# Kernel optimization log

Hardware: AMD Instinct MI355X
Metric: run time of the kernel (lower is better)

Reference implementation:

```python
import jax, jax.numpy as jnp
import numpy as np
from jax import lax

V, D, H = 32000, 512, 512  # vocab, embedding_dim, hidden_size (must match for the DxD matmul chain)
B, T, A = 64, 256, 4       # batch, sentence len, aspect len
EPS = 1e-5


def setup_inputs() -> dict:
    key = jax.random.key(0)
    ks = jax.random.split(key, 12)
    sc = 0.05
    return {
        "x": jax.random.randint(ks[0], (B, T), 0, V),
        "s": jax.random.randint(ks[1], (B, A), 0, V),
        "embed": jax.random.normal(ks[2], (V, D), jnp.float32) * sc,
        "W_ih": jax.random.normal(ks[3], (4 * H, D), jnp.float32) * sc,
        "W_hh": jax.random.normal(ks[4], (4 * H, H), jnp.float32) * sc,
        "b_lstm": jax.random.normal(ks[5], (4 * H,), jnp.float32) * sc,
        "w_y": jax.random.normal(ks[6], (D, D), jnp.float32) * sc,
        "w_t": jax.random.normal(ks[7], (D, D), jnp.float32) * sc,
        "w_p": jax.random.normal(ks[8], (D, D), jnp.float32) * sc,
        "w_x": jax.random.normal(ks[9], (D, D), jnp.float32) * sc,
        "w_f": jax.random.normal(ks[10], (D, D), jnp.float32) * sc,
        "b_f": jax.random.normal(ks[11], (D,), jnp.float32) * sc,
    }


def _lstm(emb, W_ih, W_hh, b):
    # emb: [B, T, D] -> hidden states [B, T, H]; PyTorch gate order i,f,g,o
    Bx = emb.shape[0]
    Hh = W_hh.shape[1]
    h0 = jnp.zeros((Bx, Hh), emb.dtype)
    c0 = jnp.zeros((Bx, Hh), emb.dtype)

    def step(carry, x_t):
        h, c = carry
        z = x_t @ W_ih.T + h @ W_hh.T + b  # [B, 4H]
        i, f, g, o = jnp.split(z, 4, axis=-1)
        c = jax.nn.sigmoid(f) * c + jax.nn.sigmoid(i) * jnp.tanh(g)
        h = jax.nn.sigmoid(o) * jnp.tanh(c)
        return (h, c), h

    _, hs = lax.scan(step, (h0, c0), jnp.swapaxes(emb, 0, 1))
    return jnp.swapaxes(hs, 0, 1)  # [B, T, H]


def reference(x, s, embed, W_ih, W_hh, b_lstm, w_y, w_t, w_p, w_x, w_f, b_f):
    # 1) embed + LSTM over the sentence
    emb = embed[x]                      # [B, T, D]
    Hs = _lstm(emb, W_ih, W_hh, b_lstm)  # [B, T, H]

    # 2) aspect: embed, batch-normalize per feature, sum over aspect tokens
    s_emb = embed[s]                    # [B, A, D]
    mu = s_emb.mean(axis=(0, 1))
    var = s_emb.var(axis=(0, 1))
    s_norm = ((s_emb - mu) * lax.rsqrt(var + EPS)).sum(axis=1)  # [B, D]

    # 3) FFT circular correlation: m_t = ifft(fft(h_t) * conj(fft(s))).real
    Hf = jnp.fft.fft(Hs, axis=-1)                      # [B, T, D] complex
    Sf = jnp.conj(jnp.fft.fft(s_norm, axis=-1))        # [B, D]
    m = jnp.fft.ifft(Hf * Sf[:, None, :], axis=-1).real.astype(Hs.dtype)  # [B, T, D]

    # 4) attention chain
    Y = jnp.tanh(jnp.einsum('de,bte->btd', w_y, m))            # [B, T, D]
    alpha = jax.nn.softmax(jnp.einsum('de,bte->btd', w_t, Y), axis=1)  # softmax over time
    r = jnp.einsum('btd,btd->bd', alpha, Hs)                   # [B, D]
    h_star = jnp.tanh(r @ w_p.T + Hs[:, -1] @ w_x.T)           # [B, D]
    return jax.nn.softmax(h_star @ w_f.T + b_f, axis=-1)       # [B, D]
```

## Files before the change

### kernel.cpp

```cpp
#include <hip/hip_runtime.h>


typedef __bf16 bf16x8 __attribute__((ext_vector_type(8)));
typedef float f32x4 __attribute__((ext_vector_type(4)));

#define B_ 64
#define T_ 256
#define D_ 512
#define H4 2048

__device__ __forceinline__ unsigned short f2bf(float f) {
    unsigned u = __float_as_uint(f);
    u += 0x7fffu + ((u >> 16) & 1u);
    return (unsigned short)(u >> 16);
}
__device__ __forceinline__ float bf2f(unsigned short x) {
    return __uint_as_float(((unsigned)x) << 16);
}
__device__ __forceinline__ float bf2f_lo(unsigned u) { return __uint_as_float(u << 16); }
__device__ __forceinline__ float bf2f_hi(unsigned u) { return __uint_as_float(u & 0xffff0000u); }

__device__ __forceinline__ float frcp(float x) { return __builtin_amdgcn_rcpf(x); }
__device__ __forceinline__ float fast_sigmoid(float x) {
    return frcp(1.f + __expf(-x));
}
__device__ __forceinline__ float fast_tanh(float x) {
    return 1.f - 2.f * frcp(1.f + __expf(2.f * x));
}

__global__ __launch_bounds__(256)
void prep_kernel(const int* __restrict__ x,
                 const int* __restrict__ s,
                 const float* __restrict__ embed,
                 const float* __restrict__ Wih,
                 const float* __restrict__ wy,
                 const float* __restrict__ wt,
                 unsigned short* __restrict__ Wcat,
                 unsigned short* __restrict__ Ebf,
                 uint4* __restrict__ Hs4,
                 float* __restrict__ s_norm,
                 int use_ebf)
{
    __shared__ int sidx[256];
    const int bid = blockIdx.x;
    const int tid = threadIdx.x;

    if (bid < 2048) {
        const int i = (bid * 256 + tid) * 2;
        uint4 v = {0xFFFFFFFFu, 0xFFFFFFFFu, 0xFFFFFFFFu, 0xFFFFFFFFu};
        Hs4[i] = v;
        Hs4[i + 1] = v;
    } else if (bid < 3584) {
        const int i = ((bid - 2048) * 256 + tid) * 4;
        const float* src; int off;
        if (i < 1048576)      { src = Wih; off = 0; }
        else if (i < 1310720) { src = wy;  off = 1048576; }
        else                  { src = wt;  off = 1310720; }
        float4 v = *(const float4*)(src + (i - off));
        unsigned short o[4] __attribute__((aligned(8)));
        o[0] = f2bf(v.x); o[1] = f2bf(v.y); o[2] = f2bf(v.z); o[3] = f2bf(v.w);
        *(unsigned long long*)(Wcat + i) = *(const unsigned long long*)o;
    } else if (bid < 7680) {
        if (!use_ebf) return;
        const long i = ((long)(bid - 3584) * 256 + tid) * 8;
        const int row = (int)(i >> 9);
        const int col = (int)(i & 511);
        const float* src = embed + (long)x[row] * 512 + col;
        float4 u0 = *(const float4*)(src);
        float4 u1 = *(const float4*)(src + 4);
        unsigned short o[8] __attribute__((aligned(16)));
        o[0] = f2bf(u0.x); o[1] = f2bf(u0.y); o[2] = f2bf(u0.z); o[3] = f2bf(u0.w);
        o[4] = f2bf(u1.x); o[5] = f2bf(u1.y); o[6] = f2bf(u1.z); o[7] = f2bf(u1.w);
        *(uint4*)(Ebf + i) = *(const uint4*)o;
    } else {
        const int d = (bid - 7680) * 256 + tid;
        sidx[tid] = s[tid];
        __syncthreads();
        float sum = 0.f, sq = 0.f;
        for (int i = 0; i < 256; i++) {
            float v = embed[(long)sidx[i] * D_ + d];
            sum += v; sq += v * v;
        }
        float mu = sum * (1.f / 256.f);
        float var = sq * (1.f / 256.f) - mu * mu;
        float rstd = rsqrtf(var + 1e-5f);
        for (int b = 0; b < 64; b++) {
            float acc = 0.f;
            #pragma unroll
            for (int a = 0; a < 4; a++) {
                acc += embed[(long)sidx[b * 4 + a] * D_ + d] - mu;
            }
            s_norm[b * D_ + d] = acc * rstd;
        }
    }
}

__global__ __launch_bounds__(256)
void gemm_bt(const void* __restrict__ Abase, int a_f32,
             const int* __restrict__ gather_idx,
             const unsigned short* __restrict__ Bmat_h,
             const float* __restrict__ circ_src,
             const float* __restrict__ bias,
             unsigned short* __restrict__ outb,
             float* __restrict__ outf,
             int N, int K,
             long A_bstride, long out_bstride,
             int act)
{
    __shared__ __align__(16) unsigned short Asm[128 * 40];
    __shared__ __align__(16) unsigned short Bsm[128 * 40];

    const int bz = blockIdx.z;
    const int tile_n = blockIdx.x * 128;
    const int tile_m = blockIdx.y * 128;
    const int tid = threadIdx.x;
    const int lane = tid & 63;
    const int w = tid >> 6;
    const int wm = (w >> 1) * 64;
    const int wn = (w & 1) * 64;

    const int srow = tid >> 1;
    const int skc = (tid & 1) * 16;

    const float* arow_f = nullptr;
    const unsigned short* arow_h = nullptr;
    if (a_f32) {
        const float* Af = (const float*)Abase;
        if (gather_idx) arow_f = Af + (long)gather_idx[tile_m + srow] * K;
        else            arow_f = Af + (long)bz * A_bstride + (long)(tile_m + srow) * K;
    } else {
        arow_h = (const unsigned short*)Abase + (long)bz * A_bstride + (long)(tile_m + srow) * K;
    }
    const unsigned short* brow_h = nullptr;
    const float* csrc = nullptr;
    if (circ_src) csrc = circ_src + bz * 512;
    else brow_h = Bmat_h + (long)(tile_n + srow) * K;

    f32x4 zero4 = {0.f, 0.f, 0.f, 0.f};
    f32x4 acc[4][4];
    #pragma unroll
    for (int mi = 0; mi < 4; mi++)
        #pragma unroll
        for (int ni = 0; ni < 4; ni++) acc[mi][ni] = zero4;

    const int fr = lane & 15;
    const int fq = (lane >> 4) * 8;

    for (int kc = 0; kc < K; kc += 32) {
        __syncthreads();
        if (a_f32) {
            float4 u0 = *(const float4*)(arow_f + kc + skc);
            float4 u1 = *(const float4*)(arow_f + kc + skc + 4);
            float4 u2 = *(const float4*)(arow_f + kc + skc + 8);
            float4 u3 = *(const float4*)(arow_f + kc + skc + 12);
            unsigned short tmp[16] __attribute__((aligned(16)));
            tmp[0] = f2bf(u0.x); tmp[1] = f2bf(u0.y); tmp[2]  = f2bf(u0.z); tmp[3]  = f2bf(u0.w);
            tmp[4] = f2bf(u1.x); tmp[5] = f2bf(u1.y); tmp[6]  = f2bf(u1.z); tmp[7]  = f2bf(u1.w);
            tmp[8] = f2bf(u2.x); tmp[9] = f2bf(u2.y); tmp[10] = f2bf(u2.z); tmp[11] = f2bf(u2.w);
            tmp[12] = f2bf(u3.x); tmp[13] = f2bf(u3.y); tmp[14] = f2bf(u3.z); tmp[15] = f2bf(u3.w);
            *(uint4*)&Asm[srow * 40 + skc]     = *(const uint4*)tmp;
            *(uint4*)&Asm[srow * 40 + skc + 8] = *(const uint4*)(tmp + 8);
        } else {
            *(uint4*)&Asm[srow * 40 + skc]     = *(const uint4*)(arow_h + kc + skc);
            *(uint4*)&Asm[srow * 40 + skc + 8] = *(const uint4*)(arow_h + kc + skc + 8);
        }
        if (csrc) {
            unsigned short tmp[16] __attribute__((aligned(16)));
            int n_abs = tile_n + srow;
            #pragma unroll
            for (int j = 0; j < 16; j++) {
                int k_abs = kc + skc + j;
                tmp[j] = f2bf(csrc[(k_abs - n_abs) & 511]);
            }
            *(uint4*)&Bsm[srow * 40 + skc]     = *(const uint4*)tmp;
            *(uint4*)&Bsm[srow * 40 + skc + 8] = *(const uint4*)(tmp + 8);
        } else {
            *(uint4*)&Bsm[srow * 40 + skc]     = *(const uint4*)(brow_h + kc + skc);
            *(uint4*)&Bsm[srow * 40 + skc + 8] = *(const uint4*)(brow_h + kc + skc + 8);
        }
        __syncthreads();
        bf16x8 av[4], bv[4];
        #pragma unroll
        for (int mi = 0; mi < 4; mi++)
            av[mi] = *(const bf16x8*)&Asm[(wm + mi * 16 + fr) * 40 + fq];
        #pragma unroll
        for (int ni = 0; ni < 4; ni++)
            bv[ni] = *(const bf16x8*)&Bsm[(wn + ni * 16 + fr) * 40 + fq];
        #pragma unroll
        for (int mi = 0; mi < 4; mi++)
            #pragma unroll
            for (int ni = 0; ni < 4; ni++)
                acc[mi][ni] = __builtin_amdgcn_mfma_f32_16x16x32_bf16(
                    av[mi], bv[ni], acc[mi][ni], 0, 0, 0);
    }

    #pragma unroll
    for (int mi = 0; mi < 4; mi++) {
        #pragma unroll
        for (int ni = 0; ni < 4; ni++) {
            #pragma unroll
            for (int rg = 0; rg < 4; rg++) {
                int row = tile_m + wm + mi * 16 + (lane >> 4) * 4 + rg;
                int col = tile_n + wn + ni * 16 + (lane & 15);
                float v = acc[mi][ni][rg];
                if (bias) v += bias[col];
                if (act == 1) v = fast_tanh(v);
                long oidx = (long)bz * out_bstride + (long)row * N + col;
                if (outb) outb[oidx] = f2bf(v);
                else outf[oidx] = v;
            }
        }
    }
}

#define WSTRIDE 520
#define SENT 0xFFFFFFFFu
#define ZL(g,r,d) zl[((g)*8+(r))*65+(d)]

__global__ __launch_bounds__(512, 2)
void persistent_lstm(const float* __restrict__ Whh,
                     const unsigned short* __restrict__ Zx,
                     unsigned int* __restrict__ Hsu)
{
    __shared__ __align__(16) unsigned short hsm[16 * WSTRIDE];
    __shared__ float zl[4 * 8 * 65];

    const int cq  = blockIdx.x & 7;
    const int nbp = blockIdx.x >> 3;
    const int tid = threadIdx.x;
    const int w = tid >> 6;
    const int lane = tid & 63;
    const int fr = lane & 15;
    const int fq = (lane >> 4) * 8;
    const int g = w >> 1;
    const int f = w & 1;

    bf16x8 wfrag[2][16];
    #pragma unroll
    for (int n = 0; n < 2; n++) {
        const float* wrow = Whh + (long)(g * 512 + nbp * 64 + f * 32 + n * 16 + fr) * 512;
        #pragma unroll
        for (int c = 0; c < 16; c++) {
            int k0 = c * 32 + fq;
            float4 u0 = *(const float4*)(wrow + k0);
            float4 u1 = *(const float4*)(wrow + k0 + 4);
            unsigned short tmp[8] __attribute__((aligned(16)));
            tmp[0] = f2bf(u0.x); tmp[1] = f2bf(u0.y); tmp[2] = f2bf(u0.z); tmp[3] = f2bf(u0.w);
            tmp[4] = f2bf(u1.x); tmp[5] = f2bf(u1.y); tmp[6] = f2bf(u1.z); tmp[7] = f2bf(u1.w);
            wfrag[n][c] = *(const bf16x8*)tmp;
        }
    }

    for (int i = tid; i < 16 * WSTRIDE / 2; i += 512)
        ((unsigned*)hsm)[i] = 0;

    int st_r[4], st_dp[4];
    #pragma unroll
    for (int k = 0; k < 4; k++) {
        int idx = k * 512 + tid;
        st_r[k] = idx >> 8;
        st_dp[k] = idx & 255;
    }

    const int grow = (tid & 255) >> 5;
    const int d0 = (tid & 31) * 2;
    const int b_own = cq * 8 + grow;
    const int dg = nbp * 64 + d0;
    float ca = 0.f, cb = 0.f;

    f32x4 zero4 = {0.f, 0.f, 0.f, 0.f};

    for (int t = 0; t < T_; t++) {
        unsigned zi_u = 0, zf_u = 0, zg_u = 0, zo_u = 0;
        if (tid < 256) {
            const long zb = ((long)b_own * T_ + t) * H4 + dg;
            zi_u = *(const unsigned*)&Zx[zb + 0 * 512];
            zf_u = *(const unsigned*)&Zx[zb + 1 * 512];
            zg_u = *(const unsigned*)&Zx[zb + 2 * 512];
            zo_u = *(const unsigned*)&Zx[zb + 3 * 512];
        }

        f32x4 an0 = zero4, an1 = zero4;
        if (t > 0) {
            unsigned vv[4];
            long ad[4];
            #pragma unroll
            for (int k = 0; k < 4; k++) {
                ad[k] = ((long)(cq * 8 + st_r[k]) * T_ + (t - 1)) * 256 + st_dp[k];
                vv[k] = __hip_atomic_load(Hsu + ad[k], __ATOMIC_RELAXED,
                                          __HIP_MEMORY_SCOPE_AGENT);
            }
            while (true) {
                bool pend = false;
                #pragma unroll
                for (int k = 0; k < 4; k++) pend |= (vv[k] == SENT);
                if (!__ballot(pend)) break;
                #pragma unroll
                for (int k = 0; k < 4; k++) {
                    vv[k] = __hip_atomic_load(Hsu + ad[k], __ATOMIC_RELAXED,
                                              __HIP_MEMORY_SCOPE_AGENT);
                }
            }
            #pragma unroll
            for (int k = 0; k < 4; k++) {
                *(unsigned*)&hsm[st_r[k] * WSTRIDE + st_dp[k] * 2] = vv[k];
            }
            __syncthreads();
            const unsigned short* arow = hsm + fr * WSTRIDE;
            f32x4 a0[4] = {zero4, zero4, zero4, zero4};
            f32x4 a1[4] = {zero4, zero4, zero4, zero4};
            #pragma unroll
            for (int c = 0; c < 16; c += 4) {
                bf16x8 x0 = *(const bf16x8*)(arow + (c + 0) * 32 + fq);
                bf16x8 x1 = *(const bf16x8*)(arow + (c + 1) * 32 + fq);
                bf16x8 x2 = *(const bf16x8*)(arow + (c + 2) * 32 + fq);
                bf16x8 x3 = *(const bf16x8*)(arow + (c + 3) * 32 + fq);
                a0[0] = __builtin_amdgcn_mfma_f32_16x16x32_bf16(x0, wfrag[0][c + 0], a0[0], 0, 0, 0);
                a0[1] = __builtin_amdgcn_mfma_f32_16x16x32_bf16(x1, wfrag[0][c + 1], a0[1], 0, 0, 0);
                a0[2] = __builtin_amdgcn_mfma_f32_16x16x32_bf16(x2, wfrag[0][c + 2], a0[2], 0, 0, 0);
                a0[3] = __builtin_amdgcn_mfma_f32_16x16x32_bf16(x3, wfrag[0][c + 3], a0[3], 0, 0, 0);
                a1[0] = __builtin_amdgcn_mfma_f32_16x16x32_bf16(x0, wfrag[1][c + 0], a1[0], 0, 0, 0);
                a1[1] = __builtin_amdgcn_mfma_f32_16x16x32_bf16(x1, wfrag[1][c + 1], a1[1], 0, 0, 0);
                a1[2] = __builtin_amdgcn_mfma_f32_16x16x32_bf16(x2, wfrag[1][c + 2], a1[2], 0, 0, 0);
                a1[3] = __builtin_amdgcn_mfma_f32_16x16x32_bf16(x3, wfrag[1][c + 3], a1[3], 0, 0, 0);
            }
            an0 = (a0[0] + a0[1]) + (a0[2] + a0[3]);
            an1 = (a1[0] + a1[1]) + (a1[2] + a1[3]);
        }
        if (lane < 32) {
            const int rb = (lane >> 4) * 4;
            const int cl = f * 32 + (lane & 15);
            #pragma unroll
            for (int rg = 0; rg < 4; rg++) {
                ZL(g, rb + rg, cl)      = an0[rg];
                ZL(g, rb + rg, cl + 16) = an1[rg];
            }
        }
        __syncthreads();
        if (tid < 256) {
            float zi0 = ZL(0, grow, d0)     + bf2f_lo(zi_u);
            float zi1 = ZL(0, grow, d0 + 1) + bf2f_hi(zi_u);
            float zf0 = ZL(1, grow, d0)     + bf2f_lo(zf_u);
            float zf1 = ZL(1, grow, d0 + 1) + bf2f_hi(zf_u);
            float zg0 = ZL(2, grow, d0)     + bf2f_lo(zg_u);
            float zg1 = ZL(2, grow, d0 + 1) + bf2f_hi(zg_u);
            float zo0 = ZL(3, grow, d0)     + bf2f_lo(zo_u);
            float zo1 = ZL(3, grow, d0 + 1) + bf2f_hi(zo_u);

            ca = fast_sigmoid(zf0) * ca + fast_sigmoid(zi0) * fast_tanh(zg0);
            cb = fast_sigmoid(zf1) * cb + fast_sigmoid(zi1) * fast_tanh(zg1);
            float h0 = fast_sigmoid(zo0) * fast_tanh(ca);
            float h1 = fast_sigmoid(zo1) * fast_tanh(cb);

            unsigned hp = (unsigned)f2bf(h0) | ((unsigned)f2bf(h1) << 16);
            __hip_atomic_store(Hsu + ((long)b_own * T_ + t) * 256 + nbp * 32 + (tid & 31),
                               hp, __ATOMIC_RELAXED, __HIP_MEMORY_SCOPE_AGENT);
        }
    }
}

__global__ __launch_bounds__(256)
void tail_kernel(const float* __restrict__ apre,
                 const unsigned short* __restrict__ Hs,
                 const float* __restrict__ w_p,
                 const float* __restrict__ w_x,
                 const float* __restrict__ w_f,
                 const float* __restrict__ b_f,
                 float* __restrict__ out)
{
    __shared__ __align__(16) float apc[16 * 512];
    __shared__ __align__(16) unsigned short hc[16 * 512];
    __shared__ float rs[512];
    __shared__ float hts[512];
    __shared__ float hsr[512];
    __shared__ float lg[512];
    __shared__ float red[8];

    const int b = blockIdx.x, tid = threadIdx.x;
    const int d1 = tid + 256;
    const float* apb = apre + (long)b * T_ * D_;
    const unsigned short* hpb = Hs + (long)b * T_ * D_;

    float mx0 = -3.0e38f, sm0 = 0.f, ac0 = 0.f;
    float mx1 = -3.0e38f, sm1 = 0.f, ac1 = 0.f;

    for (int t0 = 0; t0 < T_; t0 += 16) {
        __syncthreads();
        for (int idx = tid; idx < 16 * 128; idx += 256) {
            int rr = idx >> 7, cc = (idx & 127) * 4;
            *(float4*)&apc[rr * 512 + cc] = *(const float4*)(apb + (long)(t0 + rr) * 512 + cc);
        }
        for (int idx = tid; idx < 16 * 64; idx += 256) {
            int rr = idx >> 6, cc = (idx & 63) * 8;
            *(uint4*)&hc[rr * 512 + cc] = *(const uint4*)(hpb + (long)(t0 + rr) * 512 + cc);
        }
        __syncthreads();
        #pragma unroll
        for (int i = 0; i < 16; i++) {
            float v0 = apc[i * 512 + tid];
            float h0 = bf2f(hc[i * 512 + tid]);
            if (v0 > mx0) {
                float fct = __expf(mx0 - v0);
                sm0 = sm0 * fct + 1.f;
                ac0 = ac0 * fct + h0;
                mx0 = v0;
            } else {
                float e = __expf(v0 - mx0);
                sm0 += e;
                ac0 += e * h0;
            }
            float v1 = apc[i * 512 + d1];
            float h1 = bf2f(hc[i * 512 + d1]);
            if (v1 > mx1) {
                float fct = __expf(mx1 - v1);
                sm1 = sm1 * fct + 1.f;
                ac1 = ac1 * fct + h1;
                mx1 = v1;
            } else {
                float e = __expf(v1 - mx1);
                sm1 += e;
                ac1 += e * h1;
            }
        }
    }
    rs[tid] = ac0 / sm0;
    rs[d1]  = ac1 / sm1;
    const long hlast = ((long)b * T_ + (T_ - 1)) * D_;
    hts[tid] = bf2f(Hs[hlast + tid]);
    hts[d1]  = bf2f(Hs[hlast + d1]);
    __syncthreads();

    for (int d = tid; d < 512; d += 256) {
        const float* wp = w_p + (long)d * D_;
        const float* wx = w_x + (long)d * D_;
        float acc = 0.f;
        for (int e = 0; e < 512; e += 4) {
            float4 p1 = *(const float4*)(wp + e);
            float4 p2 = *(const float4*)(wx + e);
            acc += p1.x * rs[e] + p1.y * rs[e + 1] + p1.z * rs[e + 2] + p1.w * rs[e + 3];
            acc += p2.x * hts[e] + p2.y * hts[e + 1] + p2.z * hts[e + 2] + p2.w * hts[e + 3];
        }
        hsr[d] = fast_tanh(acc);
    }
    __syncthreads();

    for (int d = tid; d < 512; d += 256) {
        const float* wr = w_f + (long)d * D_;
        float acc = b_f[d];
        for (int e = 0; e < 512; e += 4) {
            float4 p = *(const float4*)(wr + e);
            acc += p.x * hsr[e] + p.y * hsr[e + 1] + p.z * hsr[e + 2] + p.w * hsr[e + 3];
        }
        lg[d] = acc;
    }
    __syncthreads();
    float m0 = fmaxf(lg[tid], lg[d1]);
    for (int off = 32; off > 0; off >>= 1) m0 = fmaxf(m0, __shfl_down(m0, off, 64));
    if ((tid & 63) == 0) red[tid >> 6] = m0;
    __syncthreads();
    float bmax = fmaxf(fmaxf(red[0], red[1]), fmaxf(red[2], red[3]));
    float e0 = __expf(lg[tid] - bmax);
    float e1 = __expf(lg[d1] - bmax);
    float s0 = e0 + e1;
    for (int off = 32; off > 0; off >>= 1) s0 += __shfl_down(s0, off, 64);
    if ((tid & 63) == 0) red[4 + (tid >> 6)] = s0;
    __syncthreads();
    float inv = 1.f / (red[4] + red[5] + red[6] + red[7]);
    out[b * D_ + tid] = e0 * inv;
    out[b * D_ + d1]  = e1 * inv;
}

extern "C" void kernel_launch(void* const* d_in, const int* in_sizes, int n_in,
                              void* d_out, int out_size, void* d_ws, size_t ws_size,
                              hipStream_t stream)
{
    (void)in_sizes; (void)n_in; (void)out_size;

    const int* x = (const int*)d_in[0];
    const int* s = (const int*)d_in[1];
    const float* embed  = (const float*)d_in[2];
    const float* W_ih   = (const float*)d_in[3];
    const float* W_hh   = (const float*)d_in[4];
    const float* b_lstm = (const float*)d_in[5];
    const float* w_y = (const float*)d_in[6];
    const float* w_t = (const float*)d_in[7];
    const float* w_p = (const float*)d_in[8];
    const float* w_x = (const float*)d_in[9];
    const float* w_f = (const float*)d_in[10];
    const float* b_f = (const float*)d_in[11];

    char* ws = (char*)d_ws;
    unsigned short* Zx   = (unsigned short*)(ws + 0);
    float*          apre = (float*)(ws + 0);
    unsigned short* mbuf = (unsigned short*)(ws + 33554432);
    unsigned short* Ybuf = (unsigned short*)(ws + 50331648);
    unsigned short* Hs   = (unsigned short*)(ws + 67108864);
    float* s_norm = (float*)(ws + 86114304);
    unsigned short* Wcat = (unsigned short*)(ws + 86507520);
    unsigned short* Wih_bf = Wcat;
    unsigned short* wy_bf  = Wcat + 1048576;
    unsigned short* wt_bf  = Wcat + 1310720;
    unsigned short* Ebf  = (unsigned short*)(ws + 89653248);
    const int use_ebf = (ws_size >= (size_t)89653248 + 16777216u);

    prep_kernel<<<dim3(7682), dim3(256), 0, stream>>>(
        x, s, embed, W_ih, w_y, w_t, Wcat, Ebf, (uint4*)Hs, s_norm, use_ebf);

    if (use_ebf)
        gemm_bt<<<dim3(16, 128, 1), dim3(256), 0, stream>>>(
            Ebf, 0, nullptr, Wih_bf, nullptr, b_lstm, Zx, nullptr,
            2048, 512, 0L, 0L, 0);
    else
        gemm_bt<<<dim3(16, 128, 1), dim3(256), 0, stream>>>(
            embed, 1, x, Wih_bf, nullptr, b_lstm, Zx, nullptr,
            2048, 512, 0L, 0L, 0);

    persistent_lstm<<<dim3(64), dim3(512), 0, stream>>>(
        W_hh, Zx, (unsigned int*)Hs);


    gemm_bt<<<dim3(4, 2, 64), dim3(256), 0, stream>>>(
        Hs, 0, nullptr, nullptr, s_norm, nullptr, mbuf, nullptr,
        512, 512, (long)(T_ * D_), (long)(T_ * D_), 0);

    gemm_bt<<<dim3(4, 128, 1), dim3(256), 0, stream>>>(
        mbuf, 0, nullptr, wy_bf, nullptr, nullptr, Ybuf, nullptr,
        512, 512, 0L, 0L, 1);

    gemm_bt<<<dim3(4, 128, 1), dim3(256), 0, stream>>>(
        Ybuf, 0, nullptr, wt_bf, nullptr, nullptr, nullptr, apre,
        512, 512, 0L, 0L, 0);

    tail_kernel<<<dim3(64), dim3(256), 0, stream>>>(
        apre, Hs, w_p, w_x, w_f, b_f, (float*)d_out);
}
```

Before: 967.7 us.

## Fuse input-projection GEMM into persistent LSTM launch with sentinel-flagged overlap

Merges the W_ih input-projection GEMM and the persistent LSTM recurrence into one launch. The first 64 blocks run the recurrence and the remaining blocks compute Zx tiles, laid out so that earlier time steps come first. Zx is pre-filled with a sentinel value, and the LSTM blocks spin on atomic loads until the Zx entries they need have been written. The aim is to hide the projection GEMM behind the serial recurrence. In exchange it adds polling overhead and a fill pass, and it depends on the 64 LSTM blocks being scheduled and co-resident first, which risks deadlock if they are not.

```diff
diff --git a/kernel.cpp b/kernel.cpp
--- a/kernel.cpp
+++ b/kernel.cpp
@@ -8,6 +8,7 @@
 #define T_ 256
 #define D_ 512
 #define H4 2048
+#define SENT 0xFFFFFFFFu
 
 __device__ __forceinline__ unsigned short f2bf(float f) {
     unsigned u = __float_as_uint(f);
@@ -26,6 +27,9 @@
 }
 __device__ __forceinline__ float fast_tanh(float x) {
     return 1.f - 2.f * frcp(1.f + __expf(2.f * x));
+}
+__device__ __forceinline__ unsigned ald(const unsigned* p) {
+    return __hip_atomic_load(p, __ATOMIC_RELAXED, __HIP_MEMORY_SCOPE_AGENT);
 }
 
 __global__ __launch_bounds__(256)
@@ -38,6 +42,7 @@
                  unsigned short* __restrict__ Wcat,
                  unsigned short* __restrict__ Ebf,
                  uint4* __restrict__ Hs4,
+                 uint4* __restrict__ Zx4,
                  float* __restrict__ s_norm,
                  int use_ebf)
 {
@@ -47,7 +52,7 @@
 
     if (bid < 2048) {
         const int i = (bid * 256 + tid) * 2;
-        uint4 v = {0xFFFFFFFFu, 0xFFFFFFFFu, 0xFFFFFFFFu, 0xFFFFFFFFu};
+        uint4 v = {SENT, SENT, SENT, SENT};
         Hs4[i] = v;
         Hs4[i + 1] = v;
     } else if (bid < 3584) {
@@ -72,7 +77,7 @@
         o[0] = f2bf(u0.x); o[1] = f2bf(u0.y); o[2] = f2bf(u0.z); o[3] = f2bf(u0.w);
         o[4] = f2bf(u1.x); o[5] = f2bf(u1.y); o[6] = f2bf(u1.z); o[7] = f2bf(u1.w);
         *(uint4*)(Ebf + i) = *(const uint4*)o;
-    } else {
+    } else if (bid < 7682) {
         const int d = (bid - 7680) * 256 + tid;
         sidx[tid] = s[tid];
         __syncthreads();
@@ -92,6 +97,11 @@
             }
             s_norm[b * D_ + d] = acc * rstd;
         }
+    } else {
+        const long i = ((long)(bid - 7682) * 256 + tid) * 2;
+        uint4 v = {SENT, SENT, SENT, SENT};
+        Zx4[i] = v;
+        Zx4[i + 1] = v;
     }
 }
 
@@ -214,24 +224,108 @@
 }
 
 #define WSTRIDE 520
-#define SENT 0xFFFFFFFFu
 #define ZL(g,r,d) zl[((g)*8+(r))*65+(d)]
 
 __global__ __launch_bounds__(512, 2)
-void persistent_lstm(const float* __restrict__ Whh,
-                     const unsigned short* __restrict__ Zx,
-                     unsigned int* __restrict__ Hsu)
+void lstm_g1(const float* __restrict__ Whh,
+             unsigned int* __restrict__ Zxu,
+             unsigned int* __restrict__ Hsu,
+             const void* __restrict__ Abase, int a_f32,
+             const int* __restrict__ xg,
+             const unsigned short* __restrict__ Wih_bf,
+             const float* __restrict__ b_lstm)
 {
-    __shared__ __align__(16) unsigned short hsm[16 * WSTRIDE];
-    __shared__ float zl[4 * 8 * 65];
+    __shared__ __align__(16) char smem[25088];
+    const int tid = threadIdx.x;
+    const int lane = tid & 63;
+    const int w = tid >> 6;
+    const int fr = lane & 15;
+    const int fq = (lane >> 4) * 8;
+    f32x4 zero4 = {0.f, 0.f, 0.f, 0.f};
+
+    if (blockIdx.x >= 64) {
+        unsigned short* Asm = (unsigned short*)smem;
+        unsigned short* Bsm = (unsigned short*)(smem + 10240);
+
+        const int gb = (int)blockIdx.x - 64;
+        const int bx = gb & 15;
+        const int y  = gb >> 4;
+        const int b  = y & 63;
+        const int tb = y >> 6;
+        const int tile_m = b * 256 + tb * 128;
+        const int tile_n = bx * 128;
+
+        const int srow = tid >> 2;
+        const int skc = (tid & 3) * 8;
+
+        const float* arow_f = nullptr;
+        const unsigned short* arow_h = nullptr;
+        if (a_f32) arow_f = (const float*)Abase + (long)xg[tile_m + srow] * 512;
+        else       arow_h = (const unsigned short*)Abase + (long)(tile_m + srow) * 512;
+        const unsigned short* brow_h = Wih_bf + (long)(tile_n + srow) * 512;
+
+        const int wm = (w >> 2) * 64;
+        const int wn = (w & 3) * 32;
+
+        f32x4 acc[4][2];
+        #pragma unroll
+        for (int mi = 0; mi < 4; mi++) { acc[mi][0] = zero4; acc[mi][1] = zero4; }
+
+        for (int kc = 0; kc < 512; kc += 32) {
+            __syncthreads();
+            if (a_f32) {
+                float4 u0 = *(const float4*)(arow_f + kc + skc);
+                float4 u1 = *(const float4*)(arow_f + kc + skc + 4);
+                unsigned short tmp[8] __attribute__((aligned(16)));
+                tmp[0] = f2bf(u0.x); tmp[1] = f2bf(u0.y); tmp[2] = f2bf(u0.z); tmp[3] = f2bf(u0.w);
+                tmp[4] = f2bf(u1.x); tmp[5] = f2bf(u1.y); tmp[6] = f2bf(u1.z); tmp[7] = f2bf(u1.w);
+                *(uint4*)&Asm[srow * 40 + skc] = *(const uint4*)tmp;
+            } else {
+                *(uint4*)&Asm[srow * 40 + skc] = *(const uint4*)(arow_h + kc + skc);
+            }
+            *(uint4*)&Bsm[srow * 40 + skc] = *(const uint4*)(brow_h + kc + skc);
+            __syncthreads();
+            bf16x8 av[4], bv[2];
+            #pragma unroll
+            for (int mi = 0; mi < 4; mi++)
+                av[mi] = *(const bf16x8*)&Asm[(wm + mi * 16 + fr) * 40 + fq];
+            #pragma unroll
+            for (int ni = 0; ni < 2; ni++)
+                bv[ni] = *(const bf16x8*)&Bsm[(wn + ni * 16 + fr) * 40 + fq];
+            #pragma unroll
+            for (int mi = 0; mi < 4; mi++)
+                #pragma unroll
+                for (int ni = 0; ni < 2; ni++)
+                    acc[mi][ni] = __builtin_amdgcn_mfma_f32_16x16x32_bf16(
+                        av[mi], bv[ni], acc[mi][ni], 0, 0, 0);
+        }
+
+        #pragma unroll
+        for (int mi = 0; mi < 4; mi++) {
+            #pragma unroll
+            for (int ni = 0; ni < 2; ni++) {
+                #pragma unroll
+                for (int rg = 0; rg < 4; rg++) {
+                    int row = tile_m + wm + mi * 16 + (lane >> 4) * 4 + rg;
+                    int col = tile_n + wn + ni * 16 + (lane & 15);
+                    float v = acc[mi][ni][rg] + b_lstm[col];
+                    float vx = __shfl_xor(v, 1);
+                    if (!(lane & 1)) {
+                        unsigned pk = (unsigned)f2bf(v) | ((unsigned)f2bf(vx) << 16);
+                        __hip_atomic_store(Zxu + (((long)row * 2048 + col) >> 1), pk,
+                                           __ATOMIC_RELAXED, __HIP_MEMORY_SCOPE_AGENT);
+                    }
+                }
+            }
+        }
+        return;
+    }
+
+    unsigned short* hsm = (unsigned short*)smem;
+    float* zl = (float*)(smem + 16640);
 
     const int cq  = blockIdx.x & 7;
     const int nbp = blockIdx.x >> 3;
-    const int tid = threadIdx.x;
-    const int w = tid >> 6;
-    const int lane = tid & 63;
-    const int fr = lane & 15;
-    const int fq = (lane >> 4) * 8;
     const int g = w >> 1;
     const int f = w & 1;
 
@@ -268,16 +362,24 @@
     const int dg = nbp * 64 + d0;
     float ca = 0.f, cb = 0.f;
 
-    f32x4 zero4 = {0.f, 0.f, 0.f, 0.f};
-
     for (int t = 0; t < T_; t++) {
         unsigned zi_u = 0, zf_u = 0, zg_u = 0, zo_u = 0;
         if (tid < 256) {
-            const long zb = ((long)b_own * T_ + t) * H4 + dg;
-            zi_u = *(const unsigned*)&Zx[zb + 0 * 512];
-            zf_u = *(const unsigned*)&Zx[zb + 1 * 512];
-            zg_u = *(const unsigned*)&Zx[zb + 2 * 512];
-            zo_u = *(const unsigned*)&Zx[zb + 3 * 512];
+            const long zd = (((long)b_own * T_ + t) * H4 + dg) >> 1;
+            zi_u = ald(Zxu + zd + 0 * 256);
+            zf_u = ald(Zxu + zd + 1 * 256);
+            zg_u = ald(Zxu + zd + 2 * 256);
+            zo_u = ald(Zxu + zd + 3 * 256);
+            while (true) {
+                bool pend = (zi_u == SENT) | (zf_u == SENT) |
+                            (zg_u == SENT) | (zo_u == SENT);
+                if (!__ballot(pend)) break;
+                __builtin_amdgcn_s_sleep(2);
+                zi_u = ald(Zxu + zd + 0 * 256);
+                zf_u = ald(Zxu + zd + 1 * 256);
+                zg_u = ald(Zxu + zd + 2 * 256);
+                zo_u = ald(Zxu + zd + 3 * 256);
+            }
         }
 
         f32x4 an0 = zero4, an1 = zero4;
@@ -287,8 +389,7 @@
             #pragma unroll
             for (int k = 0; k < 4; k++) {
                 ad[k] = ((long)(cq * 8 + st_r[k]) * T_ + (t - 1)) * 256 + st_dp[k];
-                vv[k] = __hip_atomic_load(Hsu + ad[k], __ATOMIC_RELAXED,
-                                          __HIP_MEMORY_SCOPE_AGENT);
+                vv[k] = ald(Hsu + ad[k]);
             }
             while (true) {
                 bool pend = false;
@@ -296,10 +397,7 @@
                 for (int k = 0; k < 4; k++) pend |= (vv[k] == SENT);
                 if (!__ballot(pend)) break;
                 #pragma unroll
-                for (int k = 0; k < 4; k++) {
-                    vv[k] = __hip_atomic_load(Hsu + ad[k], __ATOMIC_RELAXED,
-                                              __HIP_MEMORY_SCOPE_AGENT);
-                }
+                for (int k = 0; k < 4; k++) vv[k] = ald(Hsu + ad[k]);
             }
             #pragma unroll
             for (int k = 0; k < 4; k++) {
@@ -503,20 +601,18 @@
     unsigned short* Ebf  = (unsigned short*)(ws + 89653248);
     const int use_ebf = (ws_size >= (size_t)89653248 + 16777216u);
 
-    prep_kernel<<<dim3(7682), dim3(256), 0, stream>>>(
-        x, s, embed, W_ih, w_y, w_t, Wcat, Ebf, (uint4*)Hs, s_norm, use_ebf);
+    prep_kernel<<<dim3(15874), dim3(256), 0, stream>>>(
+        x, s, embed, W_ih, w_y, w_t, Wcat, Ebf, (uint4*)Hs, (uint4*)Zx,
+        s_norm, use_ebf);
 
     if (use_ebf)
-        gemm_bt<<<dim3(16, 128, 1), dim3(256), 0, stream>>>(
-            Ebf, 0, nullptr, Wih_bf, nullptr, b_lstm, Zx, nullptr,
-            2048, 512, 0L, 0L, 0);
+        lstm_g1<<<dim3(2112), dim3(512), 0, stream>>>(
+            W_hh, (unsigned int*)Zx, (unsigned int*)Hs,
+            Ebf, 0, x, Wih_bf, b_lstm);
     else
-        gemm_bt<<<dim3(16, 128, 1), dim3(256), 0, stream>>>(
-            embed, 1, x, Wih_bf, nullptr, b_lstm, Zx, nullptr,
-            2048, 512, 0L, 0L, 0);
-
-    persistent_lstm<<<dim3(64), dim3(512), 0, stream>>>(
-        W_hh, Zx, (unsigned int*)Hs);
+        lstm_g1<<<dim3(2112), dim3(512), 0, stream>>>(
+            W_hh, (unsigned int*)Zx, (unsigned int*)Hs,
+            embed, 1, x, Wih_bf, b_lstm);
 
 
     gemm_bt<<<dim3(4, 2, 64), dim3(256), 0, stream>>>(
```

After: 984.6 us. Within noise of the previous version (+1.7%).

## Split LSTM recurrent matmul over K halves per wave instead of N halves

Applied to the files above, without the earlier changes.

In the persistent LSTM kernel, each wave now computes all 64 output columns of its gate over half of the hidden dimension (K split), instead of 32 columns over the full K. Partial sums from the two K halves go to separate shared-memory slots and are added in the gate-update phase. Each wave now reads half as many h fragments from LDS per step and has more independent MFMA accumulator chains. The cost is doubled shared-memory space for partial sums, more LDS stores per step, and an extra add during gate combination.

```diff
diff --git a/kernel.cpp b/kernel.cpp
--- a/kernel.cpp
+++ b/kernel.cpp
@@ -8,6 +8,7 @@
 #define T_ 256
 #define D_ 512
 #define H4 2048
+#define SENT 0xFFFFFFFFu
 
 __device__ __forceinline__ unsigned short f2bf(float f) {
     unsigned u = __float_as_uint(f);
@@ -47,7 +48,7 @@
 
     if (bid < 2048) {
         const int i = (bid * 256 + tid) * 2;
-        uint4 v = {0xFFFFFFFFu, 0xFFFFFFFFu, 0xFFFFFFFFu, 0xFFFFFFFFu};
+        uint4 v = {SENT, SENT, SENT, SENT};
         Hs4[i] = v;
         Hs4[i + 1] = v;
     } else if (bid < 3584) {
@@ -214,8 +215,7 @@
 }
 
 #define WSTRIDE 520
-#define SENT 0xFFFFFFFFu
-#define ZL(g,r,d) zl[((g)*8+(r))*65+(d)]
+#define ZL2(kh,g,r,d) zl[((((kh)*4+(g))*8+(r))*65)+(d)]
 
 __global__ __launch_bounds__(512, 2)
 void persistent_lstm(const float* __restrict__ Whh,
@@ -223,7 +223,7 @@
                      unsigned int* __restrict__ Hsu)
 {
     __shared__ __align__(16) unsigned short hsm[16 * WSTRIDE];
-    __shared__ float zl[4 * 8 * 65];
+    __shared__ float zl[2 * 4 * 8 * 65];
 
     const int cq  = blockIdx.x & 7;
     const int nbp = blockIdx.x >> 3;
@@ -232,16 +232,16 @@
     const int lane = tid & 63;
     const int fr = lane & 15;
     const int fq = (lane >> 4) * 8;
-    const int g = w >> 1;
-    const int f = w & 1;
-
-    bf16x8 wfrag[2][16];
+    const int g  = w >> 1;
+    const int kh = w & 1;
+
+    bf16x8 wfrag[4][8];
     #pragma unroll
-    for (int n = 0; n < 2; n++) {
-        const float* wrow = Whh + (long)(g * 512 + nbp * 64 + f * 32 + n * 16 + fr) * 512;
-        #pragma unroll
-        for (int c = 0; c < 16; c++) {
-            int k0 = c * 32 + fq;
+    for (int n = 0; n < 4; n++) {
+        const float* wrow = Whh + (long)(g * 512 + nbp * 64 + n * 16 + fr) * 512;
+        #pragma unroll
+        for (int c = 0; c < 8; c++) {
+            int k0 = kh * 256 + c * 32 + fq;
             float4 u0 = *(const float4*)(wrow + k0);
             float4 u1 = *(const float4*)(wrow + k0 + 4);
             unsigned short tmp[8] __attribute__((aligned(16)));
@@ -280,7 +280,7 @@
             zo_u = *(const unsigned*)&Zx[zb + 3 * 512];
         }
 
-        f32x4 an0 = zero4, an1 = zero4;
+        f32x4 an[4] = {zero4, zero4, zero4, zero4};
         if (t > 0) {
             unsigned vv[4];
             long ad[4];
@@ -306,46 +306,44 @@
                 *(unsigned*)&hsm[st_r[k] * WSTRIDE + st_dp[k] * 2] = vv[k];
             }
             __syncthreads();
-            const unsigned short* arow = hsm + fr * WSTRIDE;
-            f32x4 a0[4] = {zero4, zero4, zero4, zero4};
-            f32x4 a1[4] = {zero4, zero4, zero4, zero4};
-            #pragma unroll
-            for (int c = 0; c < 16; c += 4) {
+            const unsigned short* arow = hsm + fr * WSTRIDE + kh * 256;
+            f32x4 acf[4][2];
+            #pragma unroll
+            for (int n = 0; n < 4; n++) { acf[n][0] = zero4; acf[n][1] = zero4; }
+            #pragma unroll
+            for (int c = 0; c < 8; c += 2) {
                 bf16x8 x0 = *(const bf16x8*)(arow + (c + 0) * 32 + fq);
                 bf16x8 x1 = *(const bf16x8*)(arow + (c + 1) * 32 + fq);
-                bf16x8 x2 = *(const bf16x8*)(arow + (c + 2) * 32 + fq);
-                bf16x8 x3 = *(const bf16x8*)(arow + (c + 3) * 32 + fq);
-                a0[0] = __builtin_amdgcn_mfma_f32_16x16x32_bf16(x0, wfrag[0][c + 0], a0[0], 0, 0, 0);
-                a0[1] = __builtin_amdgcn_mfma_f32_16x16x32_bf16(x1, wfrag[0][c + 1], a0[1], 0, 0, 0);
-                a0[2] = __builtin_amdgcn_mfma_f32_16x16x32_bf16(x2, wfrag[0][c + 2], a0[2], 0, 0, 0);
-                a0[3] = __builtin_amdgcn_mfma_f32_16x16x32_bf16(x3, wfrag[0][c + 3], a0[3], 0, 0, 0);
-                a1[0] = __builtin_amdgcn_mfma_f32_16x16x32_bf16(x0, wfrag[1][c + 0], a1[0], 0, 0, 0);
-                a1[1] = __builtin_amdgcn_mfma_f32_16x16x32_bf16(x1, wfrag[1][c + 1], a1[1], 0, 0, 0);
-                a1[2] = __builtin_amdgcn_mfma_f32_16x16x32_bf16(x2, wfrag[1][c + 2], a1[2], 0, 0, 0);
-                a1[3] = __builtin_amdgcn_mfma_f32_16x16x32_bf16(x3, wfrag[1][c + 3], a1[3], 0, 0, 0);
-            }
-            an0 = (a0[0] + a0[1]) + (a0[2] + a0[3]);
-            an1 = (a1[0] + a1[1]) + (a1[2] + a1[3]);
+                #pragma unroll
+                for (int n = 0; n < 4; n++) {
+                    acf[n][0] = __builtin_amdgcn_mfma_f32_16x16x32_bf16(x0, wfrag[n][c + 0], acf[n][0], 0, 0, 0);
+                    acf[n][1] = __builtin_amdgcn_mfma_f32_16x16x32_bf16(x1, wfrag[n][c + 1], acf[n][1], 0, 0, 0);
+                }
+            }
+            #pragma unroll
+            for (int n = 0; n < 4; n++) an[n] = acf[n][0] + acf[n][1];
         }
         if (lane < 32) {
             const int rb = (lane >> 4) * 4;
-            const int cl = f * 32 + (lane & 15);
-            #pragma unroll
-            for (int rg = 0; rg < 4; rg++) {
-                ZL(g, rb + rg, cl)      = an0[rg];
-                ZL(g, rb + rg, cl + 16) = an1[rg];
+            const int cl = lane & 15;
+            #pragma unroll
+            for (int n = 0; n < 4; n++) {
+                #pragma unroll
+                for (int rg = 0; rg < 4; rg++) {
+                    ZL2(kh, g, rb + rg, n * 16 + cl) = an[n][rg];
+                }
             }
         }
         __syncthreads();
         if (tid < 256) {
-            float zi0 = ZL(0, grow, d0)     + bf2f_lo(zi_u);
-            float zi1 = ZL(0, grow, d0 + 1) + bf2f_hi(zi_u);
-            float zf0 = ZL(1, grow, d0)     + bf2f_lo(zf_u);
-            float zf1 = ZL(1, grow, d0 + 1) + bf2f_hi(zf_u);
-            float zg0 = ZL(2, grow, d0)     + bf2f_lo(zg_u);
-            float zg1 = ZL(2, grow, d0 + 1) + bf2f_hi(zg_u);
-            float zo0 = ZL(3, grow, d0)     + bf2f_lo(zo_u);
-            float zo1 = ZL(3, grow, d0 + 1) + bf2f_hi(zo_u);
+            float zi0 = ZL2(0, 0, grow, d0)     + ZL2(1, 0, grow, d0)     + bf2f_lo(zi_u);
+            float zi1 = ZL2(0, 0, grow, d0 + 1) + ZL2(1, 0, grow, d0 + 1) + bf2f_hi(zi_u);
+            float zf0 = ZL2(0, 1, grow, d0)     + ZL2(1, 1, grow, d0)     + bf2f_lo(zf_u);
+            float zf1 = ZL2(0, 1, grow, d0 + 1) + ZL2(1, 1, grow, d0 + 1) + bf2f_hi(zf_u);
+            float zg0 = ZL2(0, 2, grow, d0)     + ZL2(1, 2, grow, d0)     + bf2f_lo(zg_u);
+            float zg1 = ZL2(0, 2, grow, d0 + 1) + ZL2(1, 2, grow, d0 + 1) + bf2f_hi(zg_u);
+            float zo0 = ZL2(0, 3, grow, d0)     + ZL2(1, 3, grow, d0)     + bf2f_lo(zo_u);
+            float zo1 = ZL2(0, 3, grow, d0 + 1) + ZL2(1, 3, grow, d0 + 1) + bf2f_hi(zo_u);
 
             ca = fast_sigmoid(zf0) * ca + fast_sigmoid(zi0) * fast_tanh(zg0);
             cb = fast_sigmoid(zf1) * cb + fast_sigmoid(zi1) * fast_tanh(zg1);
```

New measurement: 1.028 ms. +6.2%, slower.
